# Kernel optimization log

Hardware: AMD Instinct MI355X
Metric: run time of the kernel (lower is better)

Reference implementation:

```python
import jax, jax.numpy as jnp
import numpy as np

N_NODES = 100000
N_EDGES = 1200000
NUM_GRAPHS = 64
D_IN = 64
D_H = 64
D_OUT = 2
BN_EPS = 1e-5


def setup_inputs() -> dict:
    key = jax.random.key(0)
    ks = jax.random.split(key, 12)
    x = jax.random.normal(ks[0], (N_NODES, D_IN), dtype=jnp.float32)
    edge_index = jax.random.randint(ks[1], (2, N_EDGES), 0, N_NODES, dtype=jnp.int64 if jax.config.read('jax_enable_x64') else jnp.int32)
    batch = jnp.sort(jax.random.randint(ks[2], (N_NODES,), 0, NUM_GRAPHS))
    s = 1.0 / np.sqrt(D_H)
    W1 = jax.random.uniform(ks[3], (D_IN, D_H), minval=-s, maxval=s, dtype=jnp.float32)
    b1 = jnp.zeros((D_H,), jnp.float32)
    g1 = jnp.ones((D_H,), jnp.float32); be1 = jnp.zeros((D_H,), jnp.float32)
    m1 = jax.random.normal(ks[4], (D_H,), dtype=jnp.float32) * 0.1
    v1 = jax.random.uniform(ks[5], (D_H,), minval=0.5, maxval=1.5, dtype=jnp.float32)
    W2 = jax.random.uniform(ks[6], (D_H, D_H), minval=-s, maxval=s, dtype=jnp.float32)
    b2 = jnp.zeros((D_H,), jnp.float32)
    g2 = jnp.ones((D_H,), jnp.float32); be2 = jnp.zeros((D_H,), jnp.float32)
    m2 = jax.random.normal(ks[7], (D_H,), dtype=jnp.float32) * 0.1
    v2 = jax.random.uniform(ks[8], (D_H,), minval=0.5, maxval=1.5, dtype=jnp.float32)
    Wc = jax.random.uniform(ks[9], (D_H, D_OUT), minval=-s, maxval=s, dtype=jnp.float32)
    bc = jnp.zeros((D_OUT,), jnp.float32)
    return dict(x=x, edge_index=edge_index, batch=batch, W1=W1, b1=b1, g1=g1, be1=be1, m1=m1, v1=v1,
                W2=W2, b2=b2, g2=g2, be2=be2, m2=m2, v2=v2, Wc=Wc, bc=bc)


def _gcn_conv(x, src, dst, W, b):
    n = x.shape[0]
    h = x @ W  # [N, Dh]
    deg = jax.ops.segment_sum(jnp.ones_like(dst, dtype=h.dtype), dst, num_segments=n)  # includes self-loops
    dinv = jax.lax.rsqrt(jnp.maximum(deg, 1.0))
    norm = dinv[src] * dinv[dst]  # [E+N]
    msg = h[src] * norm[:, None]
    out = jax.ops.segment_sum(msg, dst, num_segments=n)
    return out + b


def _bn(x, g, be, m, v):
    return (x - m) * (g * jax.lax.rsqrt(v + BN_EPS)) + be


def reference(x, edge_index, batch, W1, b1, g1, be1, m1, v1, W2, b2, g2, be2, m2, v2, Wc, bc):
    n = x.shape[0]
    loop = jnp.arange(n, dtype=edge_index.dtype)
    src = jnp.concatenate([edge_index[0], loop])
    dst = jnp.concatenate([edge_index[1], loop])
    h = _gcn_conv(x, src, dst, W1, b1)
    h = jax.nn.relu(_bn(h, g1, be1, m1, v1))  # dropout is identity in eval
    h = _gcn_conv(h, src, dst, W2, b2)
    h = jax.nn.relu(_bn(h, g2, be2, m2, v2))
    # global mean pool over graphs
    sums = jax.ops.segment_sum(h, batch, num_segments=NUM_GRAPHS)
    cnts = jax.ops.segment_sum(jnp.ones((n,), h.dtype), batch, num_segments=NUM_GRAPHS)
    pooled = sums / jnp.maximum(cnts, 1.0)[:, None]
    return pooled @ Wc + bc
```

## Files before the change

kernel.cpp:

```cpp
#include <hip/hip_runtime.h>

#define N_NODES_C 100000
#define N_EDGES_C 1200000
#define NQUADS_C 300000
#define NUM_GRAPHS_C 64
#define D_C 64
#define BN_EPS_C 1e-5f

#define BU_SH 7
#define NB_C 782
#define PART_B 512
#define QPB 586
#define NSTRIP_C 6250

typedef unsigned short u16;
typedef unsigned int u32;

using frag_ab = __attribute__((ext_vector_type(8))) short;
using f32x4   = __attribute__((ext_vector_type(4))) float;

__device__ __forceinline__ u16 f2bf(float f) {
    u32 x = __float_as_uint(f);
    x += 0x7fffu + ((x >> 16) & 1u);
    return (u16)(x >> 16);
}
__device__ __forceinline__ float bf2f(u16 u) {
    return __uint_as_float(((u32)u) << 16);
}

__global__ void k_prepW(const float* __restrict__ W1, const float* __restrict__ W2,
                        u16* __restrict__ Wb1, u16* __restrict__ Wb2,
                        u16* __restrict__ T, u16* __restrict__ T2) {
    int i = blockIdx.x * 256 + threadIdx.x;
    if (i < 4096) {
        int n = i >> 6, k = i & 63;
        Wb1[i] = f2bf(W1[k * 64 + n]);
        Wb2[i] = f2bf(W2[k * 64 + n]);
    }
    if (i < 64) {
        T[(size_t)N_NODES_C * 64 + i] = 0;
        T2[(size_t)N_NODES_C * 64 + i] = 0;
    }
}


__global__ void __launch_bounds__(256) k_hist(const int* __restrict__ dst,
                                              u32* __restrict__ hist_all) {
    __shared__ u32 hist[NB_C];
    int b = blockIdx.x, t = threadIdx.x;
    for (int i = t; i < NB_C; i += 256) hist[i] = 0;
    __syncthreads();
    int qlo = b * QPB, qhi = qlo + QPB; if (qhi > NQUADS_C) qhi = NQUADS_C;
    const int4* d4 = (const int4*)dst;
    for (int i = qlo + t; i < qhi; i += 256) {
        int4 d = d4[i];
        atomicAdd(&hist[d.x >> BU_SH], 1u);
        atomicAdd(&hist[d.y >> BU_SH], 1u);
        atomicAdd(&hist[d.z >> BU_SH], 1u);
        atomicAdd(&hist[d.w >> BU_SH], 1u);
    }
    __syncthreads();
    for (int i = t; i < NB_C; i += 256) hist_all[(size_t)b * NB_C + i] = hist[i];
}

__global__ void __launch_bounds__(256) k_pscan(const u32* __restrict__ hist_all,
                                               u32* __restrict__ partLocal,
                                               u32* __restrict__ bucketTotal) {
    int wv = blockIdx.x * 4 + (threadIdx.x >> 6);
    int l = threadIdx.x & 63;
    if (wv >= NB_C) return;
    u32 v[8];
#pragma unroll
    for (int j = 0; j < 8; ++j) v[j] = hist_all[(size_t)(l * 8 + j) * NB_C + wv];
    u32 s = 0;
#pragma unroll
    for (int j = 0; j < 8; ++j) { u32 tv = v[j]; v[j] = s; s += tv; }
    u32 run = s;
#pragma unroll
    for (int off = 1; off < 64; off <<= 1) {
        u32 y = __shfl_up(run, off);
        if (l >= off) run += y;
    }
    u32 excl = run - s;
#pragma unroll
    for (int j = 0; j < 8; ++j)
        partLocal[(size_t)(l * 8 + j) * NB_C + wv] = excl + v[j];
    if (l == 63) bucketTotal[wv] = run;
}

__global__ void __launch_bounds__(1024) k_bscan(const u32* __restrict__ bucketTotal,
                                                u32* __restrict__ bucketStart) {
    __shared__ u32 sh[1024];
    int t = threadIdx.x;
    u32 c = (t < NB_C) ? bucketTotal[t] : 0;
    u32 val = c;
    sh[t] = val;
    __syncthreads();
#pragma unroll
    for (int off = 1; off < 1024; off <<= 1) {
        u32 y = (t >= off) ? sh[t - off] : 0;
        __syncthreads();
        val += y;
        sh[t] = val;
        __syncthreads();
    }
    if (t < NB_C) bucketStart[t] = val - c;
    if (t == 0) bucketStart[NB_C] = N_EDGES_C;
}

__global__ void __launch_bounds__(256) k_part(const int* __restrict__ src,
                                              const int* __restrict__ dst,
                                              const u32* __restrict__ partLocal,
                                              const u32* __restrict__ bucketStart,
                                              u32* __restrict__ pairs) {
    __shared__ u32 baseLDS[NB_C];
    __shared__ u32 rank[NB_C];
    int lb = ((blockIdx.x & 7) << 6) | (blockIdx.x >> 3);
    int t = threadIdx.x;
    for (int i = t; i < NB_C; i += 256) {
        baseLDS[i] = bucketStart[i] + partLocal[(size_t)lb * NB_C + i];
        rank[i] = 0;
    }
    __syncthreads();
    int qlo = lb * QPB, qhi = qlo + QPB; if (qhi > NQUADS_C) qhi = NQUADS_C;
    const int4* d4 = (const int4*)dst;
    const int4* s4 = (const int4*)src;
    for (int i = qlo + t; i < qhi; i += 256) {
        int4 d = d4[i];
        int4 s = s4[i];
        int dd[4] = {d.x, d.y, d.z, d.w};
        int ss[4] = {s.x, s.y, s.z, s.w};
#pragma unroll
        for (int k = 0; k < 4; ++k) {
            int bu = dd[k] >> BU_SH;
            u32 r = atomicAdd(&rank[bu], 1u);
            pairs[baseLDS[bu] + r] = (u32)ss[k] | ((u32)(dd[k] & 127) << 17);
        }
    }
}

__global__ void __launch_bounds__(256) k_csr(const u32* __restrict__ pairs,
                                             const u32* __restrict__ bucketStart,
                                             int* __restrict__ cnt,
                                             int* __restrict__ start,
                                             int* __restrict__ col) {
    __shared__ u32 cl[128];
    __shared__ u32 sl[128];
    __shared__ u32 rk[128];
    __shared__ int sh[256];
    int bu = blockIdx.x, t = threadIdx.x;
    int n0 = bu << BU_SH;
    u32 seg0 = bucketStart[bu], seg1 = bucketStart[bu + 1];
    if (t < 128) { cl[t] = 0; rk[t] = 0; }
    __syncthreads();
    for (u32 i = seg0 + t; i < seg1; i += 256)
        atomicAdd(&cl[pairs[i] >> 17], 1u);
    __syncthreads();
    int c = (t < 128) ? (int)cl[t] : 0;
    int val = c;
    sh[t] = val;
    __syncthreads();
#pragma unroll
    for (int off = 1; off < 128; off <<= 1) {
        int y = (t >= off) ? sh[t - off] : 0;
        __syncthreads();
        val += y;
        sh[t] = val;
        __syncthreads();
    }
    if (t < 128) {
        int node = n0 + t;
        u32 st = seg0 + (u32)(val - c);
        sl[t] = st;
        if (node < N_NODES_C) { cnt[node] = c; start[node] = (int)st; }
    }
    __syncthreads();
    for (u32 i = seg0 + t; i < seg1; i += 256) {
        u32 pr = pairs[i];
        u32 loc = pr >> 17;
        u32 r = atomicAdd(&rk[loc], 1u);
        col[sl[loc] + r] = (int)(pr & 0x1ffffu);
    }
}

__device__ __forceinline__ frag_ab cvt8(const float* __restrict__ p) {
    float4 f0 = *(const float4*)p;
    float4 f1 = *(const float4*)(p + 4);
    frag_ab r;
    r[0] = (short)f2bf(f0.x); r[1] = (short)f2bf(f0.y);
    r[2] = (short)f2bf(f0.z); r[3] = (short)f2bf(f0.w);
    r[4] = (short)f2bf(f1.x); r[5] = (short)f2bf(f1.y);
    r[6] = (short)f2bf(f1.z); r[7] = (short)f2bf(f1.w);
    return r;
}

__global__ void __launch_bounds__(256) k_xw1(
        const float* __restrict__ x, const u16* __restrict__ Wb,
        const int* __restrict__ cnt, u16* __restrict__ T) {
    int lane = threadIdx.x & 63;
    int q = lane >> 4, ln = lane & 15;
    int wave = blockIdx.x * 4 + (threadIdx.x >> 6);
    if (wave >= NSTRIP_C) return;
    frag_ab bfr[4][2];
#pragma unroll
    for (int nt = 0; nt < 4; ++nt)
#pragma unroll
        for (int kh = 0; kh < 2; ++kh)
            bfr[nt][kh] = *(const frag_ab*)(Wb + (nt * 16 + ln) * 64 + kh * 32 + q * 8);
    int r0 = wave * 16;
    const float* xr = x + (size_t)(r0 + ln) * 64;
    frag_ab a0 = cvt8(xr + q * 8);
    frag_ab a1 = cvt8(xr + 32 + q * 8);
    f32x4 acc[4];
#pragma unroll
    for (int nt = 0; nt < 4; ++nt) {
        acc[nt] = (f32x4){0.f, 0.f, 0.f, 0.f};
        acc[nt] = __builtin_amdgcn_mfma_f32_16x16x32_bf16(a0, bfr[nt][0], acc[nt], 0, 0, 0);
        acc[nt] = __builtin_amdgcn_mfma_f32_16x16x32_bf16(a1, bfr[nt][1], acc[nt], 0, 0, 0);
    }
    float di[4];
#pragma unroll
    for (int reg = 0; reg < 4; ++reg)
        di[reg] = rsqrtf((float)(cnt[r0 + q * 4 + reg] + 1));
#pragma unroll
    for (int nt = 0; nt < 4; ++nt)
#pragma unroll
        for (int reg = 0; reg < 4; ++reg)
            T[(size_t)(r0 + q * 4 + reg) * 64 + nt * 16 + ln] =
                f2bf(acc[nt][reg] * di[reg]);
}

__global__ void __launch_bounds__(256) k_g1w2(
        const u16* __restrict__ T, const int* __restrict__ col,
        const int* __restrict__ cnt, const int* __restrict__ start,
        const u16* __restrict__ Wb2,
        const float* __restrict__ b, const float* __restrict__ g,
        const float* __restrict__ be, const float* __restrict__ m,
        const float* __restrict__ v, u16* __restrict__ T2) {
    __shared__ u16 abuf[4][16][64];
    __shared__ float dibuf[4][16];
    const int ZROW = N_NODES_C;
    int lane = threadIdx.x & 63;
    int widx = threadIdx.x >> 6;
    int h = lane >> 4, c = lane & 15;
    int cbase = c << 2;
    float scv[4], c0v[4];
#pragma unroll
    for (int i = 0; i < 4; ++i) {
        float sci = g[cbase + i] * rsqrtf(v[cbase + i] + BN_EPS_C);
        scv[i] = sci;
        c0v[i] = (b[cbase + i] - m[cbase + i]) * sci + be[cbase + i];
    }
    int wave = blockIdx.x * 4 + widx;
    if (wave >= NSTRIP_C) return;
    int r0 = wave * 16;
    char* ab = (char*)&abuf[widx][0][0];

    int d0 = cnt[r0];
    int s0 = start[r0];
    int d1 = cnt[r0 + 1], s1 = start[r0 + 1];
    int cv0 = col[(size_t)(u32)s0 + lane];

    for (int i = 0; i < 16; ++i) {
        int p = r0 + i;
        int deg = __builtin_amdgcn_readfirstlane(d0);
        int cvR = cv0;
        if (i + 1 < 16) {
            cv0 = col[(size_t)(u32)s1 + lane];
            d0 = d1;
            if (i + 2 < 16) { d1 = cnt[p + 2]; s1 = start[p + 2]; }
        }
        if (deg > 63) deg = 63;
        int cv = (lane < deg) ? cvR : ((lane == deg) ? p : ZROW);
        int iters = (deg + 4) >> 2;
        float a0 = 0.f, a1 = 0.f, a2 = 0.f, a3 = 0.f;
        int sl = h;
        int j = 0;
        for (; j + 2 <= iters; j += 2) {
            int i0 = __shfl(cv, sl);
            int i1 = __shfl(cv, sl + 4);
            uint2 t0 = *(const uint2*)(T + (((size_t)(u32)i0) << 6) + (c << 2));
            uint2 t1 = *(const uint2*)(T + (((size_t)(u32)i1) << 6) + (c << 2));
            a0 += __uint_as_float(t0.x << 16); a1 += __uint_as_float(t0.x & 0xffff0000u);
            a2 += __uint_as_float(t0.y << 16); a3 += __uint_as_float(t0.y & 0xffff0000u);
            a0 += __uint_as_float(t1.x << 16); a1 += __uint_as_float(t1.x & 0xffff0000u);
            a2 += __uint_as_float(t1.y << 16); a3 += __uint_as_float(t1.y & 0xffff0000u);
            sl += 8;
        }
        if (j < iters) {
            int i0 = __shfl(cv, sl);
            uint2 t0 = *(const uint2*)(T + (((size_t)(u32)i0) << 6) + (c << 2));
            a0 += __uint_as_float(t0.x << 16); a1 += __uint_as_float(t0.x & 0xffff0000u);
            a2 += __uint_as_float(t0.y << 16); a3 += __uint_as_float(t0.y & 0xffff0000u);
        }
        a0 += __shfl_xor(a0, 16); a0 += __shfl_xor(a0, 32);
        a1 += __shfl_xor(a1, 16); a1 += __shfl_xor(a1, 32);
        a2 += __shfl_xor(a2, 16); a2 += __shfl_xor(a2, 32);
        a3 += __shfl_xor(a3, 16); a3 += __shfl_xor(a3, 32);
        float dr = rsqrtf((float)(deg + 1));
        float v0 = fmaxf(fmaf(a0 * dr, scv[0], c0v[0]), 0.f);
        float v1 = fmaxf(fmaf(a1 * dr, scv[1], c0v[1]), 0.f);
        float v2 = fmaxf(fmaf(a2 * dr, scv[2], c0v[2]), 0.f);
        float v3 = fmaxf(fmaf(a3 * dr, scv[3], c0v[3]), 0.f);
        if (h == 0) {
            u32 w0 = (u32)f2bf(v0) | ((u32)f2bf(v1) << 16);
            u32 w1 = (u32)f2bf(v2) | ((u32)f2bf(v3) << 16);
            int boff = i * 128 + ((c * 8) ^ ((i & 7) << 4));
            *(uint2*)(ab + boff) = make_uint2(w0, w1);
            if (c == 0) dibuf[widx][i] = dr;
        }
    }

    int q = h, ln = c;
    frag_ab bfr[4][2];
#pragma unroll
    for (int nt = 0; nt < 4; ++nt)
#pragma unroll
        for (int kh = 0; kh < 2; ++kh)
            bfr[nt][kh] = *(const frag_ab*)(Wb2 + (nt * 16 + ln) * 64 + kh * 32 + q * 8);
    int sw = (ln & 7) << 4;
    frag_ab fa0 = *(const frag_ab*)(ab + ln * 128 + ((q * 16) ^ sw));
    frag_ab fa1 = *(const frag_ab*)(ab + ln * 128 + ((64 + q * 16) ^ sw));
    f32x4 acc[4];
#pragma unroll
    for (int nt = 0; nt < 4; ++nt) {
        acc[nt] = (f32x4){0.f, 0.f, 0.f, 0.f};
        acc[nt] = __builtin_amdgcn_mfma_f32_16x16x32_bf16(fa0, bfr[nt][0], acc[nt], 0, 0, 0);
        acc[nt] = __builtin_amdgcn_mfma_f32_16x16x32_bf16(fa1, bfr[nt][1], acc[nt], 0, 0, 0);
    }
    float di[4];
#pragma unroll
    for (int reg = 0; reg < 4; ++reg)
        di[reg] = dibuf[widx][q * 4 + reg];
#pragma unroll
    for (int nt = 0; nt < 4; ++nt)
#pragma unroll
        for (int reg = 0; reg < 4; ++reg)
            T2[(size_t)(r0 + q * 4 + reg) * 64 + nt * 16 + ln] =
                f2bf(acc[nt][reg] * di[reg]);
}

__global__ void __launch_bounds__(256) k_gather2(
        const u16* __restrict__ T, const int* __restrict__ col,
        const int* __restrict__ cnt, const int* __restrict__ start,
        const float* __restrict__ b, const float* __restrict__ g,
        const float* __restrict__ be, const float* __restrict__ m,
        const float* __restrict__ v, const int* __restrict__ batch,
        float* __restrict__ pooled) {
    const int ZROW = N_NODES_C;
    int lane = threadIdx.x & 63;
    int h = lane >> 4, c = lane & 15;
    int cbase = c << 2;
    int wave = blockIdx.x * 4 + (threadIdx.x >> 6);
    int nwaves = gridDim.x * 4;
    float scv[4], c0v[4];
#pragma unroll
    for (int i = 0; i < 4; ++i) {
        float sci = g[cbase + i] * rsqrtf(v[cbase + i] + BN_EPS_C);
        scv[i] = sci;
        c0v[i] = (b[cbase + i] - m[cbase + i]) * sci + be[cbase + i];
    }
    const int chunk = (N_NODES_C + nwaves - 1) / nwaves;
    int p0 = wave * chunk;
    int p1 = p0 + chunk; if (p1 > N_NODES_C) p1 = N_NODES_C;
    if (p0 >= p1) return;

    float psum = 0.f; int curg = -1;

    int d0 = cnt[p0];
    int s0 = start[p0];
    int d1 = 0, s1 = 0;
    if (p0 + 1 < p1) { d1 = cnt[p0 + 1]; s1 = start[p0 + 1]; }
    int cv0 = col[(size_t)(u32)s0 + lane];

    for (int p = p0; p < p1; ++p) {
        int deg = __builtin_amdgcn_readfirstlane(d0);
        int cvR = cv0;
        if (p + 1 < p1) {
            cv0 = col[(size_t)(u32)s1 + lane];
            d0 = d1;
            if (p + 2 < p1) { d1 = cnt[p + 2]; s1 = start[p + 2]; }
        }
        if (deg > 63) deg = 63;
        int cv = (lane < deg) ? cvR : ((lane == deg) ? p : ZROW);
        int iters = (deg + 4) >> 2;
        float a0 = 0.f, a1 = 0.f, a2 = 0.f, a3 = 0.f;
        int sl = h;
        int j = 0;
        for (; j + 2 <= iters; j += 2) {
            int i0 = __shfl(cv, sl);
            int i1 = __shfl(cv, sl + 4);
            uint2 t0 = *(const uint2*)(T + (((size_t)(u32)i0) << 6) + (c << 2));
            uint2 t1 = *(const uint2*)(T + (((size_t)(u32)i1) << 6) + (c << 2));
            a0 += __uint_as_float(t0.x << 16); a1 += __uint_as_float(t0.x & 0xffff0000u);
            a2 += __uint_as_float(t0.y << 16); a3 += __uint_as_float(t0.y & 0xffff0000u);
            a0 += __uint_as_float(t1.x << 16); a1 += __uint_as_float(t1.x & 0xffff0000u);
            a2 += __uint_as_float(t1.y << 16); a3 += __uint_as_float(t1.y & 0xffff0000u);
            sl += 8;
        }
        if (j < iters) {
            int i0 = __shfl(cv, sl);
            uint2 t0 = *(const uint2*)(T + (((size_t)(u32)i0) << 6) + (c << 2));
            a0 += __uint_as_float(t0.x << 16); a1 += __uint_as_float(t0.x & 0xffff0000u);
            a2 += __uint_as_float(t0.y << 16); a3 += __uint_as_float(t0.y & 0xffff0000u);
        }
        a0 += __shfl_xor(a0, 16); a0 += __shfl_xor(a0, 32);
        a1 += __shfl_xor(a1, 16); a1 += __shfl_xor(a1, 32);
        a2 += __shfl_xor(a2, 16); a2 += __shfl_xor(a2, 32);
        a3 += __shfl_xor(a3, 16); a3 += __shfl_xor(a3, 32);
        float dr = rsqrtf((float)(deg + 1));
        float asel = (h & 2) ? ((h & 1) ? a3 : a2) : ((h & 1) ? a1 : a0);
        float scl  = (h & 2) ? ((h & 1) ? scv[3] : scv[2]) : ((h & 1) ? scv[1] : scv[0]);
        float c0l  = (h & 2) ? ((h & 1) ? c0v[3] : c0v[2]) : ((h & 1) ? c0v[1] : c0v[0]);
        float vh = fmaxf(fmaf(asel * dr, scl, c0l), 0.f);
        int gg = batch[p];
        if (gg != curg) {
            if (curg >= 0) atomicAdd(&pooled[curg * 64 + cbase + h], psum);
            curg = gg; psum = 0.f;
        }
        psum += vh;
    }
    if (curg >= 0) atomicAdd(&pooled[curg * 64 + cbase + h], psum);
}

__global__ void k_final(const float* __restrict__ pooled, const int* __restrict__ batch,
                        const float* __restrict__ Wc, const float* __restrict__ bc,
                        float* __restrict__ out) {
    __shared__ float sp[64 * 65];
    __shared__ int sub[64];
    int t = threadIdx.x;
    for (int i = t; i < 4096; i += 256) sp[(i >> 6) * 65 + (i & 63)] = pooled[i];
    if (t < 64) {
        int lo = 0, hi = N_NODES_C;
        while (lo < hi) { int mid = (lo + hi) >> 1; if (batch[mid] > t) hi = mid; else lo = mid + 1; }
        sub[t] = lo;
    }
    __syncthreads();
    if (t < 64) {
        int gi = t;
        int lb = gi ? sub[gi - 1] : 0;
        int cntg = sub[gi] - lb;
        float inv = 1.0f / fmaxf((float)cntg, 1.0f);
        float a0 = 0.f, a1 = 0.f;
#pragma unroll 8
        for (int f = 0; f < 64; ++f) {
            float p = sp[gi * 65 + f];
            a0 = fmaf(p, Wc[f * 2 + 0], a0);
            a1 = fmaf(p, Wc[f * 2 + 1], a1);
        }
        out[gi * 2 + 0] = a0 * inv + bc[0];
        out[gi * 2 + 1] = a1 * inv + bc[1];
    }
}

extern "C" void kernel_launch(void* const* d_in, const int* in_sizes, int n_in,
                              void* d_out, int out_size, void* d_ws, size_t ws_size,
                              hipStream_t stream) {
    const float* x    = (const float*)d_in[0];
    const int*   ei   = (const int*)d_in[1];
    const int*   batch= (const int*)d_in[2];
    const float* W1 = (const float*)d_in[3];
    const float* b1 = (const float*)d_in[4];
    const float* g1 = (const float*)d_in[5];
    const float* be1= (const float*)d_in[6];
    const float* m1 = (const float*)d_in[7];
    const float* v1 = (const float*)d_in[8];
    const float* W2 = (const float*)d_in[9];
    const float* b2 = (const float*)d_in[10];
    const float* g2 = (const float*)d_in[11];
    const float* be2= (const float*)d_in[12];
    const float* m2 = (const float*)d_in[13];
    const float* v2 = (const float*)d_in[14];
    const float* Wc = (const float*)d_in[15];
    const float* bc = (const float*)d_in[16];
    float* out = (float*)d_out;

    char* ws = (char*)d_ws;
    size_t off = 0;
    auto alloc = [&](size_t bytes) {
        size_t o = off;
        off = (off + bytes + 511) & ~(size_t)511;
        return o;
    };
    size_t o_pool  = alloc((size_t)NUM_GRAPHS_C * D_C * 4);
    size_t zero_bytes = off;
    size_t o_hist  = alloc((size_t)PART_B * NB_C * 4);
    size_t o_ploc  = alloc((size_t)PART_B * NB_C * 4);
    size_t o_btot  = alloc((size_t)NB_C * 4);
    size_t o_bst   = alloc((size_t)(NB_C + 2) * 4);
    size_t o_pairs = alloc((size_t)N_EDGES_C * 4);
    size_t o_cnt   = alloc((size_t)N_NODES_C * 4);
    size_t o_start = alloc((size_t)(N_NODES_C + 64) * 4);
    size_t o_col   = alloc((size_t)(N_EDGES_C + 64) * 4);
    size_t o_wb1   = alloc(4096 * 2);
    size_t o_wb2   = alloc(4096 * 2);
    size_t o_t     = alloc((size_t)(N_NODES_C + 1) * D_C * 2);
    size_t o_t2    = alloc((size_t)(N_NODES_C + 1) * D_C * 2);
    (void)ws_size; (void)in_sizes; (void)n_in; (void)out_size;

    float* pooled = (float*)(ws + o_pool);
    u32*   hist   = (u32*)(ws + o_hist);
    u32*   ploc   = (u32*)(ws + o_ploc);
    u32*   btot   = (u32*)(ws + o_btot);
    u32*   bst    = (u32*)(ws + o_bst);
    u32*   pairs  = (u32*)(ws + o_pairs);
    int*   cnt    = (int*)(ws + o_cnt);
    int*   startp = (int*)(ws + o_start);
    int*   col    = (int*)(ws + o_col);
    u16*   Wb1    = (u16*)(ws + o_wb1);
    u16*   Wb2    = (u16*)(ws + o_wb2);
    u16*   T      = (u16*)(ws + o_t);
    u16*   T2     = (u16*)(ws + o_t2);

    const int* srcp = ei;
    const int* dstp = ei + N_EDGES_C;

    hipMemsetAsync(ws, 0, zero_bytes, stream);

    int gblocks = 2048;
    int mblocks = 1563;
    k_prepW<<<16, 256, 0, stream>>>(W1, W2, Wb1, Wb2, T, T2);
    k_hist<<<PART_B, 256, 0, stream>>>(dstp, hist);
    k_pscan<<<(NB_C + 3) / 4, 256, 0, stream>>>(hist, ploc, btot);
    k_bscan<<<1, 1024, 0, stream>>>(btot, bst);
    k_part<<<PART_B, 256, 0, stream>>>(srcp, dstp, ploc, bst, pairs);
    k_csr<<<NB_C, 256, 0, stream>>>(pairs, bst, cnt, startp, col);

    k_xw1<<<mblocks, 256, 0, stream>>>(x, Wb1, cnt, T);
    k_g1w2<<<mblocks, 256, 0, stream>>>(T, col, cnt, startp, Wb2,
                                        b1, g1, be1, m1, v1, T2);
    k_gather2<<<gblocks, 256, 0, stream>>>(T2, col, cnt, startp, b2, g2, be2, m2, v2,
                                           batch, pooled);
    k_final<<<1, 256, 0, stream>>>(pooled, batch, Wc, bc, out);
}
```

Baseline: 217.0 us.

## Widen gather loads to 16 bytes per lane and fold weight prep into histogram kernel

The neighbor gather in both aggregation kernels now has 8 lanes per row, each loading a uint4 (8 bf16 values), so one wave covers 8 neighbors per step instead of 4 with 8-byte loads. This halves the number of load instructions and loop iterations per node, at the cost of one more shuffle-reduction step and twice as many accumulator registers. The second-layer pooling kernel now has each lane own one fixed output column. The separate weight-conversion kernel is merged into the histogram kernel to save a launch.

```diff
diff --git a/kernel.cpp b/kernel.cpp
--- a/kernel.cpp
+++ b/kernel.cpp
@@ -24,30 +24,30 @@
     x += 0x7fffu + ((x >> 16) & 1u);
     return (u16)(x >> 16);
 }
-__device__ __forceinline__ float bf2f(u16 u) {
-    return __uint_as_float(((u32)u) << 16);
-}
-
-__global__ void k_prepW(const float* __restrict__ W1, const float* __restrict__ W2,
-                        u16* __restrict__ Wb1, u16* __restrict__ Wb2,
-                        u16* __restrict__ T, u16* __restrict__ T2) {
-    int i = blockIdx.x * 256 + threadIdx.x;
-    if (i < 4096) {
-        int n = i >> 6, k = i & 63;
-        Wb1[i] = f2bf(W1[k * 64 + n]);
-        Wb2[i] = f2bf(W2[k * 64 + n]);
-    }
-    if (i < 64) {
-        T[(size_t)N_NODES_C * 64 + i] = 0;
-        T2[(size_t)N_NODES_C * 64 + i] = 0;
-    }
-}
+__device__ __forceinline__ float blo(u32 u) { return __uint_as_float(u << 16); }
+__device__ __forceinline__ float bhi(u32 u) { return __uint_as_float(u & 0xffff0000u); }
 
 
 __global__ void __launch_bounds__(256) k_hist(const int* __restrict__ dst,
-                                              u32* __restrict__ hist_all) {
+                                              u32* __restrict__ hist_all,
+                                              const float* __restrict__ W1,
+                                              const float* __restrict__ W2,
+                                              u16* __restrict__ Wb1,
+                                              u16* __restrict__ Wb2,
+                                              u16* __restrict__ T,
+                                              u16* __restrict__ T2) {
     __shared__ u32 hist[NB_C];
     int b = blockIdx.x, t = threadIdx.x;
+    int gi = b * 256 + t;
+    if (gi < 4096) {
+        int n = gi >> 6, k = gi & 63;
+        Wb1[gi] = f2bf(W1[k * 64 + n]);
+        Wb2[gi] = f2bf(W2[k * 64 + n]);
+    }
+    if (gi < 64) {
+        T[(size_t)N_NODES_C * 64 + gi] = 0;
+        T2[(size_t)N_NODES_C * 64 + gi] = 0;
+    }
     for (int i = t; i < NB_C; i += 256) hist[i] = 0;
     __syncthreads();
     int qlo = b * QPB, qhi = qlo + QPB; if (qhi > NQUADS_C) qhi = NQUADS_C;
@@ -230,6 +230,40 @@
                 f2bf(acc[nt][reg] * di[reg]);
 }
 
+#define GATHER_NODE(OUT0,OUT1,OUT2,OUT3,OUT4,OUT5,OUT6,OUT7)               \
+    float OUT0 = 0.f, OUT1 = 0.f, OUT2 = 0.f, OUT3 = 0.f;                  \
+    float OUT4 = 0.f, OUT5 = 0.f, OUT6 = 0.f, OUT7 = 0.f;                  \
+    {                                                                      \
+        int iters = (deg + 8) >> 3;                                        \
+        int sl = h;                                                        \
+        int j = 0;                                                         \
+        for (; j + 2 <= iters; j += 2) {                                   \
+            int i0 = __shfl(cv, sl);                                       \
+            int i1 = __shfl(cv, sl + 8);                                   \
+            uint4 t0 = *(const uint4*)(T + (((size_t)(u32)i0) << 6) + (c << 3)); \
+            uint4 t1 = *(const uint4*)(T + (((size_t)(u32)i1) << 6) + (c << 3)); \
+            OUT0 += blo(t0.x); OUT1 += bhi(t0.x); OUT2 += blo(t0.y); OUT3 += bhi(t0.y); \
+            OUT4 += blo(t0.z); OUT5 += bhi(t0.z); OUT6 += blo(t0.w); OUT7 += bhi(t0.w); \
+            OUT0 += blo(t1.x); OUT1 += bhi(t1.x); OUT2 += blo(t1.y); OUT3 += bhi(t1.y); \
+            OUT4 += blo(t1.z); OUT5 += bhi(t1.z); OUT6 += blo(t1.w); OUT7 += bhi(t1.w); \
+            sl += 16;                                                      \
+        }                                                                  \
+        if (j < iters) {                                                   \
+            int i0 = __shfl(cv, sl);                                       \
+            uint4 t0 = *(const uint4*)(T + (((size_t)(u32)i0) << 6) + (c << 3)); \
+            OUT0 += blo(t0.x); OUT1 += bhi(t0.x); OUT2 += blo(t0.y); OUT3 += bhi(t0.y); \
+            OUT4 += blo(t0.z); OUT5 += bhi(t0.z); OUT6 += blo(t0.w); OUT7 += bhi(t0.w); \
+        }                                                                  \
+    }                                                                      \
+    OUT0 += __shfl_xor(OUT0, 8); OUT0 += __shfl_xor(OUT0, 16); OUT0 += __shfl_xor(OUT0, 32); \
+    OUT1 += __shfl_xor(OUT1, 8); OUT1 += __shfl_xor(OUT1, 16); OUT1 += __shfl_xor(OUT1, 32); \
+    OUT2 += __shfl_xor(OUT2, 8); OUT2 += __shfl_xor(OUT2, 16); OUT2 += __shfl_xor(OUT2, 32); \
+    OUT3 += __shfl_xor(OUT3, 8); OUT3 += __shfl_xor(OUT3, 16); OUT3 += __shfl_xor(OUT3, 32); \
+    OUT4 += __shfl_xor(OUT4, 8); OUT4 += __shfl_xor(OUT4, 16); OUT4 += __shfl_xor(OUT4, 32); \
+    OUT5 += __shfl_xor(OUT5, 8); OUT5 += __shfl_xor(OUT5, 16); OUT5 += __shfl_xor(OUT5, 32); \
+    OUT6 += __shfl_xor(OUT6, 8); OUT6 += __shfl_xor(OUT6, 16); OUT6 += __shfl_xor(OUT6, 32); \
+    OUT7 += __shfl_xor(OUT7, 8); OUT7 += __shfl_xor(OUT7, 16); OUT7 += __shfl_xor(OUT7, 32);
+
 __global__ void __launch_bounds__(256) k_g1w2(
         const u16* __restrict__ T, const int* __restrict__ col,
         const int* __restrict__ cnt, const int* __restrict__ start,
@@ -242,11 +276,11 @@
     const int ZROW = N_NODES_C;
     int lane = threadIdx.x & 63;
     int widx = threadIdx.x >> 6;
-    int h = lane >> 4, c = lane & 15;
-    int cbase = c << 2;
-    float scv[4], c0v[4];
-#pragma unroll
-    for (int i = 0; i < 4; ++i) {
+    int h = lane >> 3, c = lane & 7;
+    int cbase = c << 3;
+    float scv[8], c0v[8];
+#pragma unroll
+    for (int i = 0; i < 8; ++i) {
         float sci = g[cbase + i] * rsqrtf(v[cbase + i] + BN_EPS_C);
         scv[i] = sci;
         c0v[i] = (b[cbase + i] - m[cbase + i]) * sci + be[cbase + i];
@@ -272,46 +306,29 @@
         }
         if (deg > 63) deg = 63;
         int cv = (lane < deg) ? cvR : ((lane == deg) ? p : ZROW);
-        int iters = (deg + 4) >> 2;
-        float a0 = 0.f, a1 = 0.f, a2 = 0.f, a3 = 0.f;
-        int sl = h;
-        int j = 0;
-        for (; j + 2 <= iters; j += 2) {
-            int i0 = __shfl(cv, sl);
-            int i1 = __shfl(cv, sl + 4);
-            uint2 t0 = *(const uint2*)(T + (((size_t)(u32)i0) << 6) + (c << 2));
-            uint2 t1 = *(const uint2*)(T + (((size_t)(u32)i1) << 6) + (c << 2));
-            a0 += __uint_as_float(t0.x << 16); a1 += __uint_as_float(t0.x & 0xffff0000u);
-            a2 += __uint_as_float(t0.y << 16); a3 += __uint_as_float(t0.y & 0xffff0000u);
-            a0 += __uint_as_float(t1.x << 16); a1 += __uint_as_float(t1.x & 0xffff0000u);
-            a2 += __uint_as_float(t1.y << 16); a3 += __uint_as_float(t1.y & 0xffff0000u);
-            sl += 8;
-        }
-        if (j < iters) {
-            int i0 = __shfl(cv, sl);
-            uint2 t0 = *(const uint2*)(T + (((size_t)(u32)i0) << 6) + (c << 2));
-            a0 += __uint_as_float(t0.x << 16); a1 += __uint_as_float(t0.x & 0xffff0000u);
-            a2 += __uint_as_float(t0.y << 16); a3 += __uint_as_float(t0.y & 0xffff0000u);
-        }
-        a0 += __shfl_xor(a0, 16); a0 += __shfl_xor(a0, 32);
-        a1 += __shfl_xor(a1, 16); a1 += __shfl_xor(a1, 32);
-        a2 += __shfl_xor(a2, 16); a2 += __shfl_xor(a2, 32);
-        a3 += __shfl_xor(a3, 16); a3 += __shfl_xor(a3, 32);
+        GATHER_NODE(a0, a1, a2, a3, a4, a5, a6, a7)
         float dr = rsqrtf((float)(deg + 1));
-        float v0 = fmaxf(fmaf(a0 * dr, scv[0], c0v[0]), 0.f);
-        float v1 = fmaxf(fmaf(a1 * dr, scv[1], c0v[1]), 0.f);
-        float v2 = fmaxf(fmaf(a2 * dr, scv[2], c0v[2]), 0.f);
-        float v3 = fmaxf(fmaf(a3 * dr, scv[3], c0v[3]), 0.f);
         if (h == 0) {
-            u32 w0 = (u32)f2bf(v0) | ((u32)f2bf(v1) << 16);
-            u32 w1 = (u32)f2bf(v2) | ((u32)f2bf(v3) << 16);
-            int boff = i * 128 + ((c * 8) ^ ((i & 7) << 4));
-            *(uint2*)(ab + boff) = make_uint2(w0, w1);
+            float v0 = fmaxf(fmaf(a0 * dr, scv[0], c0v[0]), 0.f);
+            float v1 = fmaxf(fmaf(a1 * dr, scv[1], c0v[1]), 0.f);
+            float v2 = fmaxf(fmaf(a2 * dr, scv[2], c0v[2]), 0.f);
+            float v3 = fmaxf(fmaf(a3 * dr, scv[3], c0v[3]), 0.f);
+            float v4 = fmaxf(fmaf(a4 * dr, scv[4], c0v[4]), 0.f);
+            float v5 = fmaxf(fmaf(a5 * dr, scv[5], c0v[5]), 0.f);
+            float v6 = fmaxf(fmaf(a6 * dr, scv[6], c0v[6]), 0.f);
+            float v7 = fmaxf(fmaf(a7 * dr, scv[7], c0v[7]), 0.f);
+            uint4 w;
+            w.x = (u32)f2bf(v0) | ((u32)f2bf(v1) << 16);
+            w.y = (u32)f2bf(v2) | ((u32)f2bf(v3) << 16);
+            w.z = (u32)f2bf(v4) | ((u32)f2bf(v5) << 16);
+            w.w = (u32)f2bf(v6) | ((u32)f2bf(v7) << 16);
+            int boff = i * 128 + ((c * 16) ^ ((i & 7) << 4));
+            *(uint4*)(ab + boff) = w;
             if (c == 0) dibuf[widx][i] = dr;
         }
     }
 
-    int q = h, ln = c;
+    int q = lane >> 4, ln = lane & 15;
     frag_ab bfr[4][2];
 #pragma unroll
     for (int nt = 0; nt < 4; ++nt)
@@ -349,17 +366,12 @@
         float* __restrict__ pooled) {
     const int ZROW = N_NODES_C;
     int lane = threadIdx.x & 63;
-    int h = lane >> 4, c = lane & 15;
-    int cbase = c << 2;
+    int h = lane >> 3, c = lane & 7;
+    int colown = (c << 3) | h;
+    float sc_own = g[colown] * rsqrtf(v[colown] + BN_EPS_C);
+    float c0_own = (b[colown] - m[colown]) * sc_own + be[colown];
     int wave = blockIdx.x * 4 + (threadIdx.x >> 6);
     int nwaves = gridDim.x * 4;
-    float scv[4], c0v[4];
-#pragma unroll
-    for (int i = 0; i < 4; ++i) {
-        float sci = g[cbase + i] * rsqrtf(v[cbase + i] + BN_EPS_C);
-        scv[i] = sci;
-        c0v[i] = (b[cbase + i] - m[cbase + i]) * sci + be[cbase + i];
-    }
     const int chunk = (N_NODES_C + nwaves - 1) / nwaves;
     int p0 = wave * chunk;
     int p1 = p0 + chunk; if (p1 > N_NODES_C) p1 = N_NODES_C;
@@ -383,44 +395,19 @@
         }
         if (deg > 63) deg = 63;
         int cv = (lane < deg) ? cvR : ((lane == deg) ? p : ZROW);
-        int iters = (deg + 4) >> 2;
-        float a0 = 0.f, a1 = 0.f, a2 = 0.f, a3 = 0.f;
-        int sl = h;
-        int j = 0;
-        for (; j + 2 <= iters; j += 2) {
-            int i0 = __shfl(cv, sl);
-            int i1 = __shfl(cv, sl + 4);
-            uint2 t0 = *(const uint2*)(T + (((size_t)(u32)i0) << 6) + (c << 2));
-            uint2 t1 = *(const uint2*)(T + (((size_t)(u32)i1) << 6) + (c << 2));
-            a0 += __uint_as_float(t0.x << 16); a1 += __uint_as_float(t0.x & 0xffff0000u);
-            a2 += __uint_as_float(t0.y << 16); a3 += __uint_as_float(t0.y & 0xffff0000u);
-            a0 += __uint_as_float(t1.x << 16); a1 += __uint_as_float(t1.x & 0xffff0000u);
-            a2 += __uint_as_float(t1.y << 16); a3 += __uint_as_float(t1.y & 0xffff0000u);
-            sl += 8;
-        }
-        if (j < iters) {
-            int i0 = __shfl(cv, sl);
-            uint2 t0 = *(const uint2*)(T + (((size_t)(u32)i0) << 6) + (c << 2));
-            a0 += __uint_as_float(t0.x << 16); a1 += __uint_as_float(t0.x & 0xffff0000u);
-            a2 += __uint_as_float(t0.y << 16); a3 += __uint_as_float(t0.y & 0xffff0000u);
-        }
-        a0 += __shfl_xor(a0, 16); a0 += __shfl_xor(a0, 32);
-        a1 += __shfl_xor(a1, 16); a1 += __shfl_xor(a1, 32);
-        a2 += __shfl_xor(a2, 16); a2 += __shfl_xor(a2, 32);
-        a3 += __shfl_xor(a3, 16); a3 += __shfl_xor(a3, 32);
+        GATHER_NODE(a0, a1, a2, a3, a4, a5, a6, a7)
         float dr = rsqrtf((float)(deg + 1));
-        float asel = (h & 2) ? ((h & 1) ? a3 : a2) : ((h & 1) ? a1 : a0);
-        float scl  = (h & 2) ? ((h & 1) ? scv[3] : scv[2]) : ((h & 1) ? scv[1] : scv[0]);
-        float c0l  = (h & 2) ? ((h & 1) ? c0v[3] : c0v[2]) : ((h & 1) ? c0v[1] : c0v[0]);
-        float vh = fmaxf(fmaf(asel * dr, scl, c0l), 0.f);
+        float asel = (h < 4) ? ((h < 2) ? (h == 0 ? a0 : a1) : (h == 2 ? a2 : a3))
+                             : ((h < 6) ? (h == 4 ? a4 : a5) : (h == 6 ? a6 : a7));
+        float vh = fmaxf(fmaf(asel * dr, sc_own, c0_own), 0.f);
         int gg = batch[p];
         if (gg != curg) {
-            if (curg >= 0) atomicAdd(&pooled[curg * 64 + cbase + h], psum);
+            if (curg >= 0) atomicAdd(&pooled[curg * 64 + colown], psum);
             curg = gg; psum = 0.f;
         }
         psum += vh;
     }
-    if (curg >= 0) atomicAdd(&pooled[curg * 64 + cbase + h], psum);
+    if (curg >= 0) atomicAdd(&pooled[curg * 64 + colown], psum);
 }
 
 __global__ void k_final(const float* __restrict__ pooled, const int* __restrict__ batch,
@@ -519,8 +506,7 @@
 
     int gblocks = 2048;
     int mblocks = 1563;
-    k_prepW<<<16, 256, 0, stream>>>(W1, W2, Wb1, Wb2, T, T2);
-    k_hist<<<PART_B, 256, 0, stream>>>(dstp, hist);
+    k_hist<<<PART_B, 256, 0, stream>>>(dstp, hist, W1, W2, Wb1, Wb2, T, T2);
     k_pscan<<<(NB_C + 3) / 4, 256, 0, stream>>>(hist, ploc, btot);
     k_bscan<<<1, 1024, 0, stream>>>(btot, bst);
     k_part<<<PART_B, 256, 0, stream>>>(srcp, dstp, ploc, bst, pairs);
```

Result: slower. 242.3 us (+11.7%).
